# Performance work log

Hardware: AMD Instinct MI355X
Metric: run time of the kernel (lower is better)

Reference implementation:

```python
import jax, jax.numpy as jnp
import numpy as np

N_NODES = 100000
N_EDGES = 50000
NNZ = 3200000
D = 32
ALPHA = 0.5


def setup_inputs() -> dict:
    key = jax.random.key(0)
    ks = jax.random.split(key, 10)
    X = jax.random.normal(ks[0], (N_NODES, D), dtype=jnp.float32)
    X0 = jax.random.normal(ks[1], (N_NODES, D), dtype=jnp.float32)
    atts = jax.random.uniform(ks[2], (NNZ, 1), dtype=jnp.float32)
    vertex = jax.random.randint(ks[3], (NNZ,), 0, N_NODES)
    edges = jnp.sort(jax.random.randint(ks[4], (NNZ,), 0, N_EDGES))
    s = 1.0 / np.sqrt(D)
    # Linear params stored as [in, out]
    W1_w = jax.random.uniform(ks[5], (D, D), jnp.float32, -s, s)
    W1_b = jnp.zeros((D,), jnp.float32)
    s2 = 1.0 / np.sqrt(2 * D)
    W2_w = jax.random.uniform(ks[6], (2 * D, D), jnp.float32, -s2, s2)
    W2_b = jnp.zeros((D,), jnp.float32)
    W_w = jax.random.uniform(ks[7], (D, D), jnp.float32, -s, s)
    W_b = jnp.zeros((D,), jnp.float32)
    return {"X": X, "X0": X0, "atts": atts,
            "W1_w": W1_w, "W1_b": W1_b, "W2_w": W2_w, "W2_b": W2_b,
            "W_w": W_w, "W_b": W_b, "vertex": vertex, "edges": edges}


def reference(X, X0, atts, W1_w, W1_b, W2_w, W2_b, W_w, W_b, vertex, edges):
    # EquivSetConv.forward (eval mode, 1-layer MLPs, aggr='add')
    N = X.shape[0]
    # W1(X) then gather to incidences: [nnz, D]
    X1 = X @ W1_w + W1_b
    Xve = X1[vertex] * atts  # atts [nnz,1] broadcasts over D (torch expand(-1,32))
    # scatter-add over hyperedges: [n_edges, D]
    Xe = jax.ops.segment_sum(Xve, edges, num_segments=N_EDGES)
    # gather back per incidence and mix with source node features
    Xev = jnp.concatenate([X[vertex], Xe[edges]], axis=-1)  # [nnz, 2D]
    Xev = Xev @ W2_w + W2_b  # [nnz, D]
    # scatter-add back to nodes
    Xv = jax.ops.segment_sum(Xev, vertex, num_segments=N)
    Xr = (1.0 - ALPHA) * Xv + ALPHA * X0
    return Xr @ W_w + W_b
```

## Files before the change

### kernel.cpp

```cpp
#include <hip/hip_runtime.h>
#include <hip/hip_fp16.h>

#define N_NODES 100000
#define N_EDGES 50000
#define NNZ     3200000
#define D       32
#define NB      782
#define BSH     7
#define BMSK    127u
#define PCAP    4480
#define SLOTS   72
#define P1_CHUNK 4096
#define P1_T     1024
#define P1_BLKS  ((NNZ + P1_CHUNK - 1) / P1_CHUNK)
#define P2_T     512

#define PRE_XH_BLKS   6250
#define PRE_SEG_BLKS  196
#define PRE_BCUR_BLK  (PRE_XH_BLKS + PRE_SEG_BLKS)
#define PRE_K0_BLK0   (PRE_BCUR_BLK + 1)
#define PRE_BLKS      (PRE_K0_BLK0 + 4)

typedef _Float16 half8 __attribute__((ext_vector_type(8)));
typedef float    f32x4 __attribute__((ext_vector_type(4)));

__device__ __forceinline__ unsigned int pkadd(unsigned int a, unsigned int b) {
    __half2 r = __hadd2(*(__half2*)&a, *(__half2*)&b);
    return *(unsigned int*)&r;
}

__global__ void k_pre(const float* __restrict__ X, unsigned int* __restrict__ XhU,
                      const int* __restrict__ edges, int* __restrict__ seg,
                      unsigned int* __restrict__ bcur,
                      const float* __restrict__ W1, const float* __restrict__ b1,
                      const float* __restrict__ W2, const float* __restrict__ b2,
                      const float* __restrict__ Ww,
                      _Float16* __restrict__ M1t, _Float16* __restrict__ A2t,
                      _Float16* __restrict__ Wt,
                      float* __restrict__ c1, float* __restrict__ c2) {
    int blk = blockIdx.x, t = threadIdx.x;
    if (blk < PRE_XH_BLKS) {
        int i = blk * 256 + t;
        float2 v = ((const float2*)X)[i];
        __half2 h = __floats2half2_rn(v.x, v.y);
        XhU[i] = *(const unsigned int*)&h;
    } else if (blk < PRE_BCUR_BLK) {
        int e = (blk - PRE_XH_BLKS) * 256 + t;
        if (e <= N_EDGES) {
            int lo = 0, hi = NNZ;
            while (lo < hi) { int mid = (lo + hi) >> 1; if (edges[mid] < e) lo = mid + 1; else hi = mid; }
            seg[e] = lo;
        }
    } else if (blk == PRE_BCUR_BLK) {
        for (int i = t; i < NB; i += 256) bcur[i] = (unsigned)(i * PCAP);
    } else {
        int k  = (blk - PRE_K0_BLK0) * 8 + (t >> 5);
        int dd = t & 31;
        float m = 0.f, a = 0.f;
#pragma unroll
        for (int j = 0; j < D; ++j) {
            m = fmaf(W1[k * D + j], W2[(D + j) * D + dd], m);
            a = fmaf(W2[k * D + j], Ww[j * D + dd], a);
        }
        M1t[dd * D + k] = (_Float16)m;
        A2t[dd * D + k] = (_Float16)(0.5f * a);
        Wt[dd * D + k]  = (_Float16)(0.5f * Ww[k * D + dd]);
        if (k == 0) {
            float cc1 = 0.f, cc2 = 0.f;
#pragma unroll
            for (int j = 0; j < D; ++j) {
                cc1 = fmaf(b1[j], W2[(D + j) * D + dd], cc1);
                cc2 = fmaf(b2[j], Ww[j * D + dd], cc2);
            }
            c1[dd] = cc1;
            c2[dd] = cc2;
        }
    }
}

__global__ __launch_bounds__(P1_T) void p1(const int* __restrict__ vertex,
                                           const int* __restrict__ edges,
                                           unsigned int* __restrict__ bcur,
                                           unsigned int* __restrict__ plist) {
    __shared__ unsigned int cnt[NB], excl[NB], cursor[NB], gbase[NB];
    __shared__ unsigned int scanb[P1_T];
    __shared__ unsigned int obuf[P1_CHUNK];
    __shared__ unsigned short obb[P1_CHUNK];
    int t = threadIdx.x;
    int c0 = blockIdx.x * P1_CHUNK;
    int cend = min(c0 + P1_CHUNK, NNZ);

    for (int i = t; i < NB; i += P1_T) cnt[i] = 0;
    __syncthreads();
    for (int i = c0 + t; i < cend; i += P1_T)
        atomicAdd(&cnt[((unsigned)vertex[i]) >> BSH], 1u);
    __syncthreads();

    unsigned int myc = (t < NB) ? cnt[t] : 0;
    scanb[t] = myc;
    __syncthreads();
    for (int off = 1; off < P1_T; off <<= 1) {
        unsigned int u = (t >= off) ? scanb[t - off] : 0;
        __syncthreads();
        scanb[t] += u;
        __syncthreads();
    }
    if (t < NB) {
        unsigned int ex = scanb[t] - myc;
        excl[t] = ex; cursor[t] = ex;
        gbase[t] = myc ? atomicAdd(&bcur[t], myc) : 0u;
    }
    __syncthreads();

    for (int i = c0 + t; i < cend; i += P1_T) {
        unsigned int v = (unsigned)vertex[i];
        unsigned int e = (unsigned)edges[i];
        unsigned int b = v >> BSH;
        unsigned int p = atomicAdd(&cursor[b], 1u);
        obuf[p] = (e << BSH) | (v & BMSK);
        obb[p]  = (unsigned short)b;
    }
    __syncthreads();

    int csize = cend - c0;
    for (int j = t; j < csize; j += P1_T) {
        unsigned int b = obb[j];
        plist[gbase[b] + (j - excl[b])] = obuf[j];
    }
}

__global__ void k2_edge(const unsigned int* __restrict__ XhU,
                        const float* __restrict__ atts,
                        const int* __restrict__ vertex,
                        const int* __restrict__ seg,
                        unsigned int* __restrict__ YeU,
                        float* __restrict__ saE) {
    int wave = threadIdx.x >> 6;
    int lane = threadIdx.x & 63;
    int e    = blockIdx.x * (blockDim.x >> 6) + wave;
    if (e >= N_EDGES) return;

    int start = seg[e];
    int len   = seg[e + 1] - start;
    int k16   = lane >> 2;
    int h4    = lane & 3;

    float a0 = 0.f, a1 = 0.f, a2 = 0.f, a3 = 0.f;
    float a4 = 0.f, a5 = 0.f, a6 = 0.f, a7 = 0.f;
    float sa = 0.f;

    for (int base = 0; base < len; base += 64) {
        int off = base + lane;
        int vv = 0; float aa = 0.f;
        if (off < len) { vv = vertex[start + off]; aa = atts[start + off]; }
#pragma unroll
        for (int g = 0; g < 4; ++g) {
            int   vk = __shfl(vv, g * 16 + k16, 64);
            float ak = __shfl(aa, g * 16 + k16, 64);
            uint4 w = *(const uint4*)(XhU + vk * 16 + h4 * 4);
            __half2 h0 = *(__half2*)&w.x, h1 = *(__half2*)&w.y;
            __half2 h2 = *(__half2*)&w.z, h3 = *(__half2*)&w.w;
            a0 = fmaf(ak, __low2float(h0), a0); a1 = fmaf(ak, __high2float(h0), a1);
            a2 = fmaf(ak, __low2float(h1), a2); a3 = fmaf(ak, __high2float(h1), a3);
            a4 = fmaf(ak, __low2float(h2), a4); a5 = fmaf(ak, __high2float(h2), a5);
            a6 = fmaf(ak, __low2float(h3), a6); a7 = fmaf(ak, __high2float(h3), a7);
            sa += ak;
        }
    }

    __half2 q0 = __floats2half2_rn(a0, a1), q1 = __floats2half2_rn(a2, a3);
    __half2 q2 = __floats2half2_rn(a4, a5), q3 = __floats2half2_rn(a6, a7);
    unsigned int u0 = *(unsigned int*)&q0, u1 = *(unsigned int*)&q1;
    unsigned int u2 = *(unsigned int*)&q2, u3 = *(unsigned int*)&q3;
#pragma unroll
    for (int m = 4; m < 64; m <<= 1) {
        u0 = pkadd(u0, __shfl_xor(u0, m, 64));
        u1 = pkadd(u1, __shfl_xor(u1, m, 64));
        u2 = pkadd(u2, __shfl_xor(u2, m, 64));
        u3 = pkadd(u3, __shfl_xor(u3, m, 64));
        sa += __shfl_xor(sa, m, 64);
    }
    if (k16 == 0) {
        uint4 w; w.x = u0; w.y = u1; w.z = u2; w.w = u3;
        *(uint4*)(YeU + e * 16 + h4 * 4) = w;
    }
    if (lane == 0) saE[e] = sa;
}

__global__ __launch_bounds__(256) void k2b(const unsigned int* __restrict__ YeU,
                                           const float* __restrict__ saE,
                                           const _Float16* __restrict__ M1t,
                                           const float* __restrict__ c1,
                                           unsigned int* __restrict__ FeU) {
    int wg = blockIdx.x * 4 + (threadIdx.x >> 6);
    if (wg >= N_EDGES / 16) return;
    int m0 = wg * 16;
    int l  = threadIdx.x & 63;
    int n  = l & 15, g = l >> 4;

    half8 af = *(const half8*)((const _Float16*)YeU + (size_t)(m0 + n) * D + g * 8);
    f32x4 z = {0.f, 0.f, 0.f, 0.f};

#pragma unroll
    for (int cb = 0; cb < 2; ++cb) {
        int ng = cb * 16 + n;
        half8 bf = *(const half8*)(M1t + ng * D + g * 8);
        f32x4 acc = __builtin_amdgcn_mfma_f32_16x16x32_f16(af, bf, z, 0, 0, 0);
        float c1n = c1[ng];
#pragma unroll
        for (int r = 0; r < 4; ++r) {
            int mr = m0 + g * 4 + r;
            float val = acc[r] + saE[mr] * c1n;
            float other = __shfl(val, l ^ 1, 64);
            if ((n & 1) == 0) {
                __half2 hv = __floats2half2_rn(val, other);
                FeU[mr * 16 + (ng >> 1)] = *(unsigned int*)&hv;
            }
        }
    }
}

__global__ __launch_bounds__(P2_T) void p2(const unsigned int* __restrict__ plist,
                                           const unsigned int* __restrict__ FeU,
                                           const unsigned int* __restrict__ bcur,
                                           unsigned int* __restrict__ SfU,
                                           unsigned int* __restrict__ nodedeg) {
    __shared__ unsigned int sbuf[128 * SLOTS];
    __shared__ unsigned int cursor[128];
    int t = threadIdx.x;
    if (t < 128) cursor[t] = 0;
    __syncthreads();

    int b = blockIdx.x;
    int base = b << BSH;
    int start = b * PCAP;
    int n = (int)bcur[b] - start;

    for (int i = t; i < n; i += P2_T) {
        unsigned int ent = plist[start + i];
        unsigned int lv = ent & BMSK;
        unsigned int p = atomicAdd(&cursor[lv], 1u);
        sbuf[lv * SLOTS + p] = ent >> BSH;
    }
    __syncthreads();

    int hw = t >> 5, lane = t & 31;
    int k8 = lane >> 2;
    int h4 = lane & 3;
    for (int r = 0; r < 8; ++r) {
        int ln = r * 16 + hw;
        int node = base + ln;
        if (node >= N_NODES) continue;
        int deg = (int)cursor[ln];
        const unsigned int* nbuf = sbuf + ln * SLOTS;

        unsigned int a0 = 0u, a1 = 0u, a2 = 0u, a3 = 0u;
        unsigned int a4 = 0u, a5 = 0u, a6 = 0u, a7 = 0u;
        for (int j0 = 0; j0 < deg; j0 += 16) {
            int iA = j0 + k8, iB = j0 + 8 + k8;
            bool vA = (iA < deg), vB = (iB < deg);
            unsigned int eA = vA ? nbuf[iA] : 0u;
            unsigned int eB = vB ? nbuf[iB] : 0u;
            uint4 wA = *(const uint4*)(FeU + eA * 16 + h4 * 4);
            uint4 wB = *(const uint4*)(FeU + eB * 16 + h4 * 4);
            if (!vA) { wA.x = 0u; wA.y = 0u; wA.z = 0u; wA.w = 0u; }
            if (!vB) { wB.x = 0u; wB.y = 0u; wB.z = 0u; wB.w = 0u; }
            a0 = pkadd(a0, wA.x); a1 = pkadd(a1, wA.y);
            a2 = pkadd(a2, wA.z); a3 = pkadd(a3, wA.w);
            a4 = pkadd(a4, wB.x); a5 = pkadd(a5, wB.y);
            a6 = pkadd(a6, wB.z); a7 = pkadd(a7, wB.w);
        }
        a0 = pkadd(a0, a4); a1 = pkadd(a1, a5);
        a2 = pkadd(a2, a6); a3 = pkadd(a3, a7);
#pragma unroll
        for (int m = 4; m < 32; m <<= 1) {
            a0 = pkadd(a0, __shfl_xor(a0, m, 32));
            a1 = pkadd(a1, __shfl_xor(a1, m, 32));
            a2 = pkadd(a2, __shfl_xor(a2, m, 32));
            a3 = pkadd(a3, __shfl_xor(a3, m, 32));
        }
        if (k8 == 0) {
            uint4 w; w.x = a0; w.y = a1; w.z = a2; w.w = a3;
            *(uint4*)(SfU + node * 16 + h4 * 4) = w;
        }
        if (lane == 0) nodedeg[node] = (unsigned)deg;
    }
}

__global__ __launch_bounds__(256) void k3(const float* __restrict__ X,
                                          const float* __restrict__ X0,
                                          const unsigned int* __restrict__ SfU,
                                          const unsigned int* __restrict__ nodedeg,
                                          const _Float16* __restrict__ A2t,
                                          const _Float16* __restrict__ Wt,
                                          const float* __restrict__ c2,
                                          const float* __restrict__ bw,
                                          float* __restrict__ out) {
    int wg = blockIdx.x * 4 + (threadIdx.x >> 6);
    if (wg >= N_NODES / 16) return;
    int m0 = wg * 16;
    int l  = threadIdx.x & 63;
    int n  = l & 15, g = l >> 4;
    int row = m0 + n;

    const float4* xr = (const float4*)(X + (size_t)row * D);
    float4 xa = xr[g * 2], xb = xr[g * 2 + 1];
    half8 xf = { (_Float16)xa.x, (_Float16)xa.y, (_Float16)xa.z, (_Float16)xa.w,
                 (_Float16)xb.x, (_Float16)xb.y, (_Float16)xb.z, (_Float16)xb.w };

    const __half2* sfp = (const __half2*)(SfU + (size_t)row * 16 + g * 4);
    const float4* x0r = (const float4*)(X0 + (size_t)row * D);
    float4 ya = x0r[g * 2], yb = x0r[g * 2 + 1];
    __half2 s0 = sfp[0], s1 = sfp[1], s2h = sfp[2], s3 = sfp[3];
    half8 tf = { (_Float16)(__low2float(s0) + ya.x),  (_Float16)(__high2float(s0) + ya.y),
                 (_Float16)(__low2float(s1) + ya.z),  (_Float16)(__high2float(s1) + ya.w),
                 (_Float16)(__low2float(s2h) + yb.x), (_Float16)(__high2float(s2h) + yb.y),
                 (_Float16)(__low2float(s3) + yb.z),  (_Float16)(__high2float(s3) + yb.w) };

    f32x4 z = {0.f, 0.f, 0.f, 0.f};
#pragma unroll
    for (int cb = 0; cb < 2; ++cb) {
        int ng = cb * 16 + n;
        half8 a2f = *(const half8*)(A2t + ng * D + g * 8);
        half8 wf  = *(const half8*)(Wt  + ng * D + g * 8);
        f32x4 acc1 = __builtin_amdgcn_mfma_f32_16x16x32_f16(xf, a2f, z, 0, 0, 0);
        f32x4 acc2 = __builtin_amdgcn_mfma_f32_16x16x32_f16(tf, wf,  z, 0, 0, 0);
        float hc2 = 0.5f * c2[ng];
        float bwn = bw[ng];
#pragma unroll
        for (int r = 0; r < 4; ++r) {
            int mr = m0 + g * 4 + r;
            float degf = (float)nodedeg[mr];
            out[(size_t)mr * D + ng] = fmaf(degf, acc1[r] + hc2, acc2[r] + bwn);
        }
    }
}

extern "C" void kernel_launch(void* const* d_in, const int* in_sizes, int n_in,
                              void* d_out, int out_size, void* d_ws, size_t ws_size,
                              hipStream_t stream) {
    const float* X      = (const float*)d_in[0];
    const float* X0     = (const float*)d_in[1];
    const float* atts   = (const float*)d_in[2];
    const float* W1w    = (const float*)d_in[3];
    const float* W1b    = (const float*)d_in[4];
    const float* W2w    = (const float*)d_in[5];
    const float* W2b    = (const float*)d_in[6];
    const float* Ww     = (const float*)d_in[7];
    const float* Wb     = (const float*)d_in[8];
    const int*   vertex = (const int*)d_in[9];
    const int*   edges  = (const int*)d_in[10];
    float*       out    = (float*)d_out;

    char* ws = (char*)d_ws;
    unsigned int* FeU     = (unsigned int*)(ws);
    unsigned int* plist   = (unsigned int*)(ws + 3200000);
    unsigned int* XhU     = (unsigned int*)(ws + 17208320);
    int*          seg     = (int*)         (ws + 23608320);
    unsigned int* bcur    = (unsigned int*)(ws + 23808512);
    unsigned int* YeU     = (unsigned int*)(ws + 23811712);
    float*        saE     = (float*)       (ws + 27011712);
    unsigned int* nodedeg = (unsigned int*)(ws + 27211712);
    _Float16*     M1t     = (_Float16*)    (ws + 27611712);
    _Float16*     A2t     = (_Float16*)    (ws + 27613760);
    _Float16*     Wt      = (_Float16*)    (ws + 27615808);
    float*        c1      = (float*)       (ws + 27617856);
    float*        c2      = (float*)       (ws + 27617984);
    unsigned int* SfU     = XhU;

    k_pre  <<<PRE_BLKS, 256, 0, stream>>>(X, XhU, edges, seg, bcur,
                                          W1w, W1b, W2w, W2b, Ww, M1t, A2t, Wt, c1, c2);
    p1     <<<P1_BLKS, P1_T, 0, stream>>>(vertex, edges, bcur, plist);
    k2_edge<<<(N_EDGES + 3) / 4, 256, 0, stream>>>(XhU, atts, vertex, seg, YeU, saE);
    k2b    <<<(N_EDGES / 16 + 3) / 4, 256, 0, stream>>>(YeU, saE, M1t, c1, FeU);
    p2     <<<NB, P2_T, 0, stream>>>(plist, FeU, bcur, SfU, nodedeg);
    k3     <<<(N_NODES / 16 + 3) / 4, 256, 0, stream>>>(X, X0, SfU, nodedeg,
                                                        A2t, Wt, c2, Wb, out);
}
```

Before: 121.8 us.

## Merge p1 with edge gather and fuse node epilogue into p2

The bucket-sort pass (p1) and the per-edge gather (k2_edge) become one launch, with the block index choosing which role each block plays, so the two independent phases run concurrently. The final node GEMM (k3) is folded into p2: per-node sums are staged in shared memory and degrees are read from the shared cursor instead of being written to and re-read from global SfU/nodedeg. This removes two launches and a global round trip. The costs are larger blocks with more shared memory, which may lower occupancy, and k_mid edge blocks reserve the p1 shared arrays they never use.

```diff
diff --git a/kernel.cpp b/kernel.cpp
--- a/kernel.cpp
+++ b/kernel.cpp
@@ -13,7 +13,10 @@
 #define P1_CHUNK 4096
 #define P1_T     1024
 #define P1_BLKS  ((NNZ + P1_CHUNK - 1) / P1_CHUNK)
+#define K2_BLKS  (N_EDGES / 16)
+#define MID_BLKS (P1_BLKS + K2_BLKS)
 #define P2_T     512
+#define SFP      20
 
 #define PRE_XH_BLKS   6250
 #define PRE_SEG_BLKS  196
@@ -78,113 +81,114 @@
     }
 }
 
-__global__ __launch_bounds__(P1_T) void p1(const int* __restrict__ vertex,
-                                           const int* __restrict__ edges,
-                                           unsigned int* __restrict__ bcur,
-                                           unsigned int* __restrict__ plist) {
+__global__ __launch_bounds__(1024) void k_mid(const int* __restrict__ vertex,
+                                              const int* __restrict__ edges,
+                                              unsigned int* __restrict__ bcur,
+                                              unsigned int* __restrict__ plist,
+                                              const unsigned int* __restrict__ XhU,
+                                              const float* __restrict__ atts,
+                                              const int* __restrict__ seg,
+                                              unsigned int* __restrict__ YeU,
+                                              float* __restrict__ saE) {
     __shared__ unsigned int cnt[NB], excl[NB], cursor[NB], gbase[NB];
     __shared__ unsigned int scanb[P1_T];
     __shared__ unsigned int obuf[P1_CHUNK];
     __shared__ unsigned short obb[P1_CHUNK];
     int t = threadIdx.x;
-    int c0 = blockIdx.x * P1_CHUNK;
-    int cend = min(c0 + P1_CHUNK, NNZ);
-
-    for (int i = t; i < NB; i += P1_T) cnt[i] = 0;
-    __syncthreads();
-    for (int i = c0 + t; i < cend; i += P1_T)
-        atomicAdd(&cnt[((unsigned)vertex[i]) >> BSH], 1u);
-    __syncthreads();
-
-    unsigned int myc = (t < NB) ? cnt[t] : 0;
-    scanb[t] = myc;
-    __syncthreads();
-    for (int off = 1; off < P1_T; off <<= 1) {
-        unsigned int u = (t >= off) ? scanb[t - off] : 0;
-        __syncthreads();
-        scanb[t] += u;
-        __syncthreads();
-    }
-    if (t < NB) {
-        unsigned int ex = scanb[t] - myc;
-        excl[t] = ex; cursor[t] = ex;
-        gbase[t] = myc ? atomicAdd(&bcur[t], myc) : 0u;
-    }
-    __syncthreads();
-
-    for (int i = c0 + t; i < cend; i += P1_T) {
-        unsigned int v = (unsigned)vertex[i];
-        unsigned int e = (unsigned)edges[i];
-        unsigned int b = v >> BSH;
-        unsigned int p = atomicAdd(&cursor[b], 1u);
-        obuf[p] = (e << BSH) | (v & BMSK);
-        obb[p]  = (unsigned short)b;
-    }
-    __syncthreads();
-
-    int csize = cend - c0;
-    for (int j = t; j < csize; j += P1_T) {
-        unsigned int b = obb[j];
-        plist[gbase[b] + (j - excl[b])] = obuf[j];
-    }
-}
-
-__global__ void k2_edge(const unsigned int* __restrict__ XhU,
-                        const float* __restrict__ atts,
-                        const int* __restrict__ vertex,
-                        const int* __restrict__ seg,
-                        unsigned int* __restrict__ YeU,
-                        float* __restrict__ saE) {
-    int wave = threadIdx.x >> 6;
-    int lane = threadIdx.x & 63;
-    int e    = blockIdx.x * (blockDim.x >> 6) + wave;
-    if (e >= N_EDGES) return;
-
-    int start = seg[e];
-    int len   = seg[e + 1] - start;
-    int k16   = lane >> 2;
-    int h4    = lane & 3;
-
-    float a0 = 0.f, a1 = 0.f, a2 = 0.f, a3 = 0.f;
-    float a4 = 0.f, a5 = 0.f, a6 = 0.f, a7 = 0.f;
-    float sa = 0.f;
-
-    for (int base = 0; base < len; base += 64) {
-        int off = base + lane;
-        int vv = 0; float aa = 0.f;
-        if (off < len) { vv = vertex[start + off]; aa = atts[start + off]; }
-#pragma unroll
-        for (int g = 0; g < 4; ++g) {
-            int   vk = __shfl(vv, g * 16 + k16, 64);
-            float ak = __shfl(aa, g * 16 + k16, 64);
-            uint4 w = *(const uint4*)(XhU + vk * 16 + h4 * 4);
-            __half2 h0 = *(__half2*)&w.x, h1 = *(__half2*)&w.y;
-            __half2 h2 = *(__half2*)&w.z, h3 = *(__half2*)&w.w;
-            a0 = fmaf(ak, __low2float(h0), a0); a1 = fmaf(ak, __high2float(h0), a1);
-            a2 = fmaf(ak, __low2float(h1), a2); a3 = fmaf(ak, __high2float(h1), a3);
-            a4 = fmaf(ak, __low2float(h2), a4); a5 = fmaf(ak, __high2float(h2), a5);
-            a6 = fmaf(ak, __low2float(h3), a6); a7 = fmaf(ak, __high2float(h3), a7);
-            sa += ak;
-        }
-    }
-
-    __half2 q0 = __floats2half2_rn(a0, a1), q1 = __floats2half2_rn(a2, a3);
-    __half2 q2 = __floats2half2_rn(a4, a5), q3 = __floats2half2_rn(a6, a7);
-    unsigned int u0 = *(unsigned int*)&q0, u1 = *(unsigned int*)&q1;
-    unsigned int u2 = *(unsigned int*)&q2, u3 = *(unsigned int*)&q3;
-#pragma unroll
-    for (int m = 4; m < 64; m <<= 1) {
-        u0 = pkadd(u0, __shfl_xor(u0, m, 64));
-        u1 = pkadd(u1, __shfl_xor(u1, m, 64));
-        u2 = pkadd(u2, __shfl_xor(u2, m, 64));
-        u3 = pkadd(u3, __shfl_xor(u3, m, 64));
-        sa += __shfl_xor(sa, m, 64);
-    }
-    if (k16 == 0) {
-        uint4 w; w.x = u0; w.y = u1; w.z = u2; w.w = u3;
-        *(uint4*)(YeU + e * 16 + h4 * 4) = w;
-    }
-    if (lane == 0) saE[e] = sa;
+
+    if (blockIdx.x < P1_BLKS) {
+        int c0 = blockIdx.x * P1_CHUNK;
+        int cend = min(c0 + P1_CHUNK, NNZ);
+
+        for (int i = t; i < NB; i += P1_T) cnt[i] = 0;
+        __syncthreads();
+        for (int i = c0 + t; i < cend; i += P1_T)
+            atomicAdd(&cnt[((unsigned)vertex[i]) >> BSH], 1u);
+        __syncthreads();
+
+        unsigned int myc = (t < NB) ? cnt[t] : 0;
+        scanb[t] = myc;
+        __syncthreads();
+        for (int off = 1; off < P1_T; off <<= 1) {
+            unsigned int u = (t >= off) ? scanb[t - off] : 0;
+            __syncthreads();
+            scanb[t] += u;
+            __syncthreads();
+        }
+        if (t < NB) {
+            unsigned int ex = scanb[t] - myc;
+            excl[t] = ex; cursor[t] = ex;
+            gbase[t] = myc ? atomicAdd(&bcur[t], myc) : 0u;
+        }
+        __syncthreads();
+
+        for (int i = c0 + t; i < cend; i += P1_T) {
+            unsigned int v = (unsigned)vertex[i];
+            unsigned int e = (unsigned)edges[i];
+            unsigned int b = v >> BSH;
+            unsigned int p = atomicAdd(&cursor[b], 1u);
+            obuf[p] = (e << BSH) | (v & BMSK);
+            obb[p]  = (unsigned short)b;
+        }
+        __syncthreads();
+
+        int csize = cend - c0;
+        for (int j = t; j < csize; j += P1_T) {
+            unsigned int b = obb[j];
+            plist[gbase[b] + (j - excl[b])] = obuf[j];
+        }
+    } else {
+        int wave = t >> 6;
+        int lane = t & 63;
+        int e    = (blockIdx.x - P1_BLKS) * 16 + wave;
+        if (e >= N_EDGES) return;
+
+        int start = seg[e];
+        int len   = seg[e + 1] - start;
+        int k16   = lane >> 2;
+        int h4    = lane & 3;
+
+        float a0 = 0.f, a1 = 0.f, a2 = 0.f, a3 = 0.f;
+        float a4 = 0.f, a5 = 0.f, a6 = 0.f, a7 = 0.f;
+        float sa = 0.f;
+
+        for (int base = 0; base < len; base += 64) {
+            int off = base + lane;
+            int vv = 0; float aa = 0.f;
+            if (off < len) { vv = vertex[start + off]; aa = atts[start + off]; }
+#pragma unroll
+            for (int g = 0; g < 4; ++g) {
+                int   vk = __shfl(vv, g * 16 + k16, 64);
+                float ak = __shfl(aa, g * 16 + k16, 64);
+                uint4 w = *(const uint4*)(XhU + vk * 16 + h4 * 4);
+                __half2 h0 = *(__half2*)&w.x, h1 = *(__half2*)&w.y;
+                __half2 h2 = *(__half2*)&w.z, h3 = *(__half2*)&w.w;
+                a0 = fmaf(ak, __low2float(h0), a0); a1 = fmaf(ak, __high2float(h0), a1);
+                a2 = fmaf(ak, __low2float(h1), a2); a3 = fmaf(ak, __high2float(h1), a3);
+                a4 = fmaf(ak, __low2float(h2), a4); a5 = fmaf(ak, __high2float(h2), a5);
+                a6 = fmaf(ak, __low2float(h3), a6); a7 = fmaf(ak, __high2float(h3), a7);
+                sa += ak;
+            }
+        }
+
+        __half2 q0 = __floats2half2_rn(a0, a1), q1 = __floats2half2_rn(a2, a3);
+        __half2 q2 = __floats2half2_rn(a4, a5), q3 = __floats2half2_rn(a6, a7);
+        unsigned int u0 = *(unsigned int*)&q0, u1 = *(unsigned int*)&q1;
+        unsigned int u2 = *(unsigned int*)&q2, u3 = *(unsigned int*)&q3;
+#pragma unroll
+        for (int m = 4; m < 64; m <<= 1) {
+            u0 = pkadd(u0, __shfl_xor(u0, m, 64));
+            u1 = pkadd(u1, __shfl_xor(u1, m, 64));
+            u2 = pkadd(u2, __shfl_xor(u2, m, 64));
+            u3 = pkadd(u3, __shfl_xor(u3, m, 64));
+            sa += __shfl_xor(sa, m, 64);
+        }
+        if (k16 == 0) {
+            uint4 w; w.x = u0; w.y = u1; w.z = u2; w.w = u3;
+            *(uint4*)(YeU + e * 16 + h4 * 4) = w;
+        }
+        if (lane == 0) saE[e] = sa;
+    }
 }
 
 __global__ __launch_bounds__(256) void k2b(const unsigned int* __restrict__ YeU,
@@ -220,12 +224,18 @@
     }
 }
 
-__global__ __launch_bounds__(P2_T) void p2(const unsigned int* __restrict__ plist,
-                                           const unsigned int* __restrict__ FeU,
-                                           const unsigned int* __restrict__ bcur,
-                                           unsigned int* __restrict__ SfU,
-                                           unsigned int* __restrict__ nodedeg) {
+__global__ __launch_bounds__(P2_T) void p2full(const unsigned int* __restrict__ plist,
+                                               const unsigned int* __restrict__ FeU,
+                                               const unsigned int* __restrict__ bcur,
+                                               const float* __restrict__ X,
+                                               const float* __restrict__ X0,
+                                               const _Float16* __restrict__ A2t,
+                                               const _Float16* __restrict__ Wt,
+                                               const float* __restrict__ c2,
+                                               const float* __restrict__ bw,
+                                               float* __restrict__ out) {
     __shared__ unsigned int sbuf[128 * SLOTS];
+    __shared__ unsigned int sfb[128 * SFP];
     __shared__ unsigned int cursor[128];
     int t = threadIdx.x;
     if (t < 128) cursor[t] = 0;
@@ -250,7 +260,7 @@
     for (int r = 0; r < 8; ++r) {
         int ln = r * 16 + hw;
         int node = base + ln;
-        if (node >= N_NODES) continue;
+        if (node >= N_NODES) { if (k8 == 0) { uint4 zz = {0,0,0,0}; *(uint4*)(&sfb[ln * SFP + h4 * 4]) = zz; } continue; }
         int deg = (int)cursor[ln];
         const unsigned int* nbuf = sbuf + ln * SLOTS;
 
@@ -281,37 +291,28 @@
         }
         if (k8 == 0) {
             uint4 w; w.x = a0; w.y = a1; w.z = a2; w.w = a3;
-            *(uint4*)(SfU + node * 16 + h4 * 4) = w;
-        }
-        if (lane == 0) nodedeg[node] = (unsigned)deg;
-    }
-}
-
-__global__ __launch_bounds__(256) void k3(const float* __restrict__ X,
-                                          const float* __restrict__ X0,
-                                          const unsigned int* __restrict__ SfU,
-                                          const unsigned int* __restrict__ nodedeg,
-                                          const _Float16* __restrict__ A2t,
-                                          const _Float16* __restrict__ Wt,
-                                          const float* __restrict__ c2,
-                                          const float* __restrict__ bw,
-                                          float* __restrict__ out) {
-    int wg = blockIdx.x * 4 + (threadIdx.x >> 6);
-    if (wg >= N_NODES / 16) return;
-    int m0 = wg * 16;
-    int l  = threadIdx.x & 63;
-    int n  = l & 15, g = l >> 4;
-    int row = m0 + n;
-
-    const float4* xr = (const float4*)(X + (size_t)row * D);
+            *(uint4*)(&sfb[ln * SFP + h4 * 4]) = w;
+        }
+    }
+    __syncthreads();
+
+    int wv = t >> 6;
+    int l  = t & 63;
+    int nn = l & 15, g = l >> 4;
+    int ln0 = wv * 16 + nn;
+    int row = base + ln0;
+    int rowc = min(row, N_NODES - 1);
+
+    const float4* xr = (const float4*)(X + (size_t)rowc * D);
     float4 xa = xr[g * 2], xb = xr[g * 2 + 1];
     half8 xf = { (_Float16)xa.x, (_Float16)xa.y, (_Float16)xa.z, (_Float16)xa.w,
                  (_Float16)xb.x, (_Float16)xb.y, (_Float16)xb.z, (_Float16)xb.w };
 
-    const __half2* sfp = (const __half2*)(SfU + (size_t)row * 16 + g * 4);
-    const float4* x0r = (const float4*)(X0 + (size_t)row * D);
+    uint4 sw = *(const uint4*)(&sfb[ln0 * SFP + g * 4]);
+    __half2 s0 = *(__half2*)&sw.x, s1 = *(__half2*)&sw.y;
+    __half2 s2h = *(__half2*)&sw.z, s3 = *(__half2*)&sw.w;
+    const float4* x0r = (const float4*)(X0 + (size_t)rowc * D);
     float4 ya = x0r[g * 2], yb = x0r[g * 2 + 1];
-    __half2 s0 = sfp[0], s1 = sfp[1], s2h = sfp[2], s3 = sfp[3];
     half8 tf = { (_Float16)(__low2float(s0) + ya.x),  (_Float16)(__high2float(s0) + ya.y),
                  (_Float16)(__low2float(s1) + ya.z),  (_Float16)(__high2float(s1) + ya.w),
                  (_Float16)(__low2float(s2h) + yb.x), (_Float16)(__high2float(s2h) + yb.y),
@@ -320,7 +321,7 @@
     f32x4 z = {0.f, 0.f, 0.f, 0.f};
 #pragma unroll
     for (int cb = 0; cb < 2; ++cb) {
-        int ng = cb * 16 + n;
+        int ng = cb * 16 + nn;
         half8 a2f = *(const half8*)(A2t + ng * D + g * 8);
         half8 wf  = *(const half8*)(Wt  + ng * D + g * 8);
         f32x4 acc1 = __builtin_amdgcn_mfma_f32_16x16x32_f16(xf, a2f, z, 0, 0, 0);
@@ -329,9 +330,12 @@
         float bwn = bw[ng];
 #pragma unroll
         for (int r = 0; r < 4; ++r) {
-            int mr = m0 + g * 4 + r;
-            float degf = (float)nodedeg[mr];
-            out[(size_t)mr * D + ng] = fmaf(degf, acc1[r] + hc2, acc2[r] + bwn);
+            int lnr = wv * 16 + g * 4 + r;
+            int mr = base + lnr;
+            if (mr < N_NODES) {
+                float degf = (float)cursor[lnr];
+                out[(size_t)mr * D + ng] = fmaf(degf, acc1[r] + hc2, acc2[r] + bwn);
+            }
         }
     }
 }
@@ -360,20 +364,16 @@
     unsigned int* bcur    = (unsigned int*)(ws + 23808512);
     unsigned int* YeU     = (unsigned int*)(ws + 23811712);
     float*        saE     = (float*)       (ws + 27011712);
-    unsigned int* nodedeg = (unsigned int*)(ws + 27211712);
-    _Float16*     M1t     = (_Float16*)    (ws + 27611712);
-    _Float16*     A2t     = (_Float16*)    (ws + 27613760);
-    _Float16*     Wt      = (_Float16*)    (ws + 27615808);
-    float*        c1      = (float*)       (ws + 27617856);
-    float*        c2      = (float*)       (ws + 27617984);
-    unsigned int* SfU     = XhU;
-
-    k_pre  <<<PRE_BLKS, 256, 0, stream>>>(X, XhU, edges, seg, bcur,
-                                          W1w, W1b, W2w, W2b, Ww, M1t, A2t, Wt, c1, c2);
-    p1     <<<P1_BLKS, P1_T, 0, stream>>>(vertex, edges, bcur, plist);
-    k2_edge<<<(N_EDGES + 3) / 4, 256, 0, stream>>>(XhU, atts, vertex, seg, YeU, saE);
-    k2b    <<<(N_EDGES / 16 + 3) / 4, 256, 0, stream>>>(YeU, saE, M1t, c1, FeU);
-    p2     <<<NB, P2_T, 0, stream>>>(plist, FeU, bcur, SfU, nodedeg);
-    k3     <<<(N_NODES / 16 + 3) / 4, 256, 0, stream>>>(X, X0, SfU, nodedeg,
-                                                        A2t, Wt, c2, Wb, out);
-}
+    _Float16*     M1t     = (_Float16*)    (ws + 27211712);
+    _Float16*     A2t     = (_Float16*)    (ws + 27213760);
+    _Float16*     Wt      = (_Float16*)    (ws + 27215808);
+    float*        c1      = (float*)       (ws + 27217856);
+    float*        c2      = (float*)       (ws + 27217984);
+
+    k_pre <<<PRE_BLKS, 256, 0, stream>>>(X, XhU, edges, seg, bcur,
+                                         W1w, W1b, W2w, W2b, Ww, M1t, A2t, Wt, c1, c2);
+    k_mid <<<MID_BLKS, 1024, 0, stream>>>(vertex, edges, bcur, plist,
+                                          XhU, atts, seg, YeU, saE);
+    k2b   <<<(K2_BLKS + 3) / 4, 256, 0, stream>>>(YeU, saE, M1t, c1, FeU);
+    p2full<<<NB, P2_T, 0, stream>>>(plist, FeU, bcur, X, X0, A2t, Wt, c2, Wb, out);
+}
```

Result: slower. 125.0 us (+2.7%).

## Fuse edge aggregation with MFMA projection and use wave-shuffle scan in bucketing

Applied to the files above, without the earlier changes.

Merges the per-edge gather/reduce kernel and the 16-edge MFMA projection kernel into one 1024-thread block that stages the reduced half-precision edge rows and attention sums in shared memory. This removes the YeU/saE round trip through global memory and one launch. Separately, the block-wide prefix scan in the bucketing kernel is replaced by a two-level wave-shuffle scan with far fewer barriers. The cost is that only one of the 16 waves does the MFMA step while the others idle, and the fused kernel uses larger blocks.

```diff
diff --git a/kernel.cpp b/kernel.cpp
--- a/kernel.cpp
+++ b/kernel.cpp
@@ -83,10 +83,11 @@
                                            unsigned int* __restrict__ bcur,
                                            unsigned int* __restrict__ plist) {
     __shared__ unsigned int cnt[NB], excl[NB], cursor[NB], gbase[NB];
-    __shared__ unsigned int scanb[P1_T];
+    __shared__ unsigned int wsum[16];
     __shared__ unsigned int obuf[P1_CHUNK];
     __shared__ unsigned short obb[P1_CHUNK];
     int t = threadIdx.x;
+    int wv = t >> 6, lane = t & 63;
     int c0 = blockIdx.x * P1_CHUNK;
     int cend = min(c0 + P1_CHUNK, NNZ);
 
@@ -97,27 +98,38 @@
     __syncthreads();
 
     unsigned int myc = (t < NB) ? cnt[t] : 0;
-    scanb[t] = myc;
-    __syncthreads();
-    for (int off = 1; off < P1_T; off <<= 1) {
-        unsigned int u = (t >= off) ? scanb[t - off] : 0;
-        __syncthreads();
-        scanb[t] += u;
-        __syncthreads();
-    }
+    unsigned int v = myc;
+#pragma unroll
+    for (int off = 1; off < 64; off <<= 1) {
+        unsigned int u = __shfl_up(v, off, 64);
+        if (lane >= off) v += u;
+    }
+    if (lane == 63) wsum[wv] = v;
+    __syncthreads();
+    if (t < 16) {
+        unsigned int x = wsum[t];
+#pragma unroll
+        for (int off = 1; off < 16; off <<= 1) {
+            unsigned int u = __shfl_up(x, off, 64);
+            if (t >= off) x += u;
+        }
+        wsum[t] = x;
+    }
+    __syncthreads();
+    unsigned int wbase = (wv == 0) ? 0u : wsum[wv - 1];
+    unsigned int ex = v + wbase - myc;
     if (t < NB) {
-        unsigned int ex = scanb[t] - myc;
         excl[t] = ex; cursor[t] = ex;
         gbase[t] = myc ? atomicAdd(&bcur[t], myc) : 0u;
     }
     __syncthreads();
 
     for (int i = c0 + t; i < cend; i += P1_T) {
-        unsigned int v = (unsigned)vertex[i];
+        unsigned int vv = (unsigned)vertex[i];
         unsigned int e = (unsigned)edges[i];
-        unsigned int b = v >> BSH;
+        unsigned int b = vv >> BSH;
         unsigned int p = atomicAdd(&cursor[b], 1u);
-        obuf[p] = (e << BSH) | (v & BMSK);
+        obuf[p] = (e << BSH) | (vv & BMSK);
         obb[p]  = (unsigned short)b;
     }
     __syncthreads();
@@ -129,16 +141,19 @@
     }
 }
 
-__global__ void k2_edge(const unsigned int* __restrict__ XhU,
-                        const float* __restrict__ atts,
-                        const int* __restrict__ vertex,
-                        const int* __restrict__ seg,
-                        unsigned int* __restrict__ YeU,
-                        float* __restrict__ saE) {
-    int wave = threadIdx.x >> 6;
-    int lane = threadIdx.x & 63;
-    int e    = blockIdx.x * (blockDim.x >> 6) + wave;
-    if (e >= N_EDGES) return;
+__global__ __launch_bounds__(1024) void k2f(const unsigned int* __restrict__ XhU,
+                                            const float* __restrict__ atts,
+                                            const int* __restrict__ vertex,
+                                            const int* __restrict__ seg,
+                                            const _Float16* __restrict__ M1t,
+                                            const float* __restrict__ c1,
+                                            unsigned int* __restrict__ FeU) {
+    __shared__ unsigned int yebuf[16][16];
+    __shared__ float sas[16];
+    int t = threadIdx.x;
+    int wave = t >> 6;
+    int lane = t & 63;
+    int e = blockIdx.x * 16 + wave;
 
     int start = seg[e];
     int len   = seg[e + 1] - start;
@@ -182,23 +197,16 @@
     }
     if (k16 == 0) {
         uint4 w; w.x = u0; w.y = u1; w.z = u2; w.w = u3;
-        *(uint4*)(YeU + e * 16 + h4 * 4) = w;
-    }
-    if (lane == 0) saE[e] = sa;
-}
-
-__global__ __launch_bounds__(256) void k2b(const unsigned int* __restrict__ YeU,
-                                           const float* __restrict__ saE,
-                                           const _Float16* __restrict__ M1t,
-                                           const float* __restrict__ c1,
-                                           unsigned int* __restrict__ FeU) {
-    int wg = blockIdx.x * 4 + (threadIdx.x >> 6);
-    if (wg >= N_EDGES / 16) return;
-    int m0 = wg * 16;
-    int l  = threadIdx.x & 63;
-    int n  = l & 15, g = l >> 4;
-
-    half8 af = *(const half8*)((const _Float16*)YeU + (size_t)(m0 + n) * D + g * 8);
+        *(uint4*)(&yebuf[wave][h4 * 4]) = w;
+    }
+    if (lane == 0) sas[wave] = sa;
+    __syncthreads();
+
+    if (wave != 0) return;
+    int m0 = blockIdx.x * 16;
+    int n  = lane & 15, g = lane >> 4;
+    const _Float16* yb = (const _Float16*)yebuf;
+    half8 af = *(const half8*)(yb + n * D + g * 8);
     f32x4 z = {0.f, 0.f, 0.f, 0.f};
 
 #pragma unroll
@@ -209,12 +217,12 @@
         float c1n = c1[ng];
 #pragma unroll
         for (int r = 0; r < 4; ++r) {
-            int mr = m0 + g * 4 + r;
-            float val = acc[r] + saE[mr] * c1n;
-            float other = __shfl(val, l ^ 1, 64);
+            int lr = g * 4 + r;
+            float val = acc[r] + sas[lr] * c1n;
+            float other = __shfl(val, lane ^ 1, 64);
             if ((n & 1) == 0) {
                 __half2 hv = __floats2half2_rn(val, other);
-                FeU[mr * 16 + (ng >> 1)] = *(unsigned int*)&hv;
+                FeU[(m0 + lr) * 16 + (ng >> 1)] = *(unsigned int*)&hv;
             }
         }
     }
@@ -358,22 +366,19 @@
     unsigned int* XhU     = (unsigned int*)(ws + 17208320);
     int*          seg     = (int*)         (ws + 23608320);
     unsigned int* bcur    = (unsigned int*)(ws + 23808512);
-    unsigned int* YeU     = (unsigned int*)(ws + 23811712);
-    float*        saE     = (float*)       (ws + 27011712);
-    unsigned int* nodedeg = (unsigned int*)(ws + 27211712);
-    _Float16*     M1t     = (_Float16*)    (ws + 27611712);
-    _Float16*     A2t     = (_Float16*)    (ws + 27613760);
-    _Float16*     Wt      = (_Float16*)    (ws + 27615808);
-    float*        c1      = (float*)       (ws + 27617856);
-    float*        c2      = (float*)       (ws + 27617984);
+    unsigned int* nodedeg = (unsigned int*)(ws + 23811712);
+    _Float16*     M1t     = (_Float16*)    (ws + 24211712);
+    _Float16*     A2t     = (_Float16*)    (ws + 24213760);
+    _Float16*     Wt      = (_Float16*)    (ws + 24215808);
+    float*        c1      = (float*)       (ws + 24217856);
+    float*        c2      = (float*)       (ws + 24217984);
     unsigned int* SfU     = XhU;
 
-    k_pre  <<<PRE_BLKS, 256, 0, stream>>>(X, XhU, edges, seg, bcur,
-                                          W1w, W1b, W2w, W2b, Ww, M1t, A2t, Wt, c1, c2);
-    p1     <<<P1_BLKS, P1_T, 0, stream>>>(vertex, edges, bcur, plist);
-    k2_edge<<<(N_EDGES + 3) / 4, 256, 0, stream>>>(XhU, atts, vertex, seg, YeU, saE);
-    k2b    <<<(N_EDGES / 16 + 3) / 4, 256, 0, stream>>>(YeU, saE, M1t, c1, FeU);
-    p2     <<<NB, P2_T, 0, stream>>>(plist, FeU, bcur, SfU, nodedeg);
-    k3     <<<(N_NODES / 16 + 3) / 4, 256, 0, stream>>>(X, X0, SfU, nodedeg,
-                                                        A2t, Wt, c2, Wb, out);
-}
+    k_pre <<<PRE_BLKS, 256, 0, stream>>>(X, XhU, edges, seg, bcur,
+                                         W1w, W1b, W2w, W2b, Ww, M1t, A2t, Wt, c1, c2);
+    p1    <<<P1_BLKS, P1_T, 0, stream>>>(vertex, edges, bcur, plist);
+    k2f   <<<N_EDGES / 16, 1024, 0, stream>>>(XhU, atts, vertex, seg, M1t, c1, FeU);
+    p2    <<<NB, P2_T, 0, stream>>>(plist, FeU, bcur, SfU, nodedeg);
+    k3    <<<(N_NODES / 16 + 3) / 4, 256, 0, stream>>>(X, X0, SfU, nodedeg,
+                                                       A2t, Wt, c2, Wb, out);
+}
```

After: 121.6 us. No clear change (-0.1%).
